# Optimization experiments

Measured on AMD Instinct MI355X. Metric: run time of the kernel, lower is better.

Reference implementation:

```python
import jax, jax.numpy as jnp
import numpy as np

N, K, D = 100000, 16, 128

def setup_inputs() -> dict:
    key = jax.random.key(0)
    k1, k2, k3, k4, k5 = jax.random.split(key, 5)
    s = 1.0 / np.sqrt(D)  # nn.Linear default init scale
    return {
        "h": jax.random.normal(k1, (N, D), dtype=jnp.float32),
        "nbr_idx": jax.random.randint(k2, (N, K), 0, N, dtype=jnp.int64),
        "nbr_w": jax.random.uniform(k3, (N, K), dtype=jnp.float32),
        "w_self": jax.random.uniform(k4, (D, D), minval=-s, maxval=s, dtype=jnp.float32),
        "w_nei": jax.random.uniform(k5, (D, D), minval=-s, maxval=s, dtype=jnp.float32),
        "ln_gamma": jnp.ones((D,), dtype=jnp.float32),
        "ln_beta": jnp.zeros((D,), dtype=jnp.float32),
    }

def layer_norm(x, gamma, beta, eps=1e-5):
    mu = jnp.mean(x, axis=-1, keepdims=True)
    var = jnp.mean(jnp.square(x - mu), axis=-1, keepdims=True)
    return (x - mu) * jax.lax.rsqrt(var + eps) * gamma + beta

def reference(h, nbr_idx, nbr_w, w_self, w_nei, ln_gamma, ln_beta):
    # gather neighbor features: [N, K, D]
    nei = h[nbr_idx]
    # weighted sum over neighbors -> [N, D]
    agg = jnp.einsum('nk,nkd->nd', nbr_w, nei)
    # dual linear (nn.Linear applies x @ W.T) + exact (erf) GELU
    out = jax.nn.gelu(h @ w_self.T + agg @ w_nei.T, approximate=False)
    # dropout is identity at inference; then LayerNorm
    return layer_norm(out, ln_gamma, ln_beta)
```

## Files before the change

kernel.cpp:

```cpp
#include <hip/hip_runtime.h>
#include <hip/hip_bf16.h>
#include <math.h>

#define DFEAT 128
#define KNBR  16
#define NPB   32
#define NTHR  128

typedef __attribute__((ext_vector_type(8))) short short8;
typedef __attribute__((ext_vector_type(4))) float f32x4;
typedef __attribute__((ext_vector_type(2))) unsigned u32x2;
typedef __attribute__((ext_vector_type(4))) unsigned u32x4;

__device__ __forceinline__ unsigned short f2bf(float x) {
    union { float f; unsigned u; } v; v.f = x;
    unsigned r = v.u + 0x7FFFu + ((v.u >> 16) & 1u);
    return (unsigned short)(r >> 16);
}
__device__ __forceinline__ float bf2f(unsigned short u) {
    union { unsigned u; float f; } v; v.u = ((unsigned)u) << 16; return v.f;
}
__device__ __forceinline__ bool detect_idx64(const int* p) {
    return ((p[1] | p[3] | p[5] | p[7] | p[9] | p[11] | p[13] | p[15]) == 0);
}

__global__ __launch_bounds__(256)
void prep_kernel(const float* __restrict__ h,
                 const float* __restrict__ wself,
                 const float* __restrict__ wnei,
                 unsigned short* __restrict__ h16,
                 unsigned short* __restrict__ wcat,
                 unsigned char* __restrict__ h8i,
                 float* __restrict__ sc,
                 int ntot8) {
    const int t = blockIdx.x * 256 + threadIdx.x;
    if (t < 4096) {
        const int base = t * 8;
        const int j = base >> 8;
        const int d0 = base & 255;
        const float* src = (d0 < DFEAT) ? (wself + j * DFEAT + d0)
                                        : (wnei  + j * DFEAT + (d0 - DFEAT));
        f32x4 a = ((const f32x4*)src)[0], b = ((const f32x4*)src)[1];
        short8 o;
        o[0] = f2bf(a[0]); o[1] = f2bf(a[1]); o[2] = f2bf(a[2]); o[3] = f2bf(a[3]);
        o[4] = f2bf(b[0]); o[5] = f2bf(b[1]); o[6] = f2bf(b[2]); o[7] = f2bf(b[3]);
        *(short8*)(wcat + base) = o;
        return;
    }
    const long u = (long)t - 4096;
    if (u >= ntot8) return;
    f32x4 a = __builtin_nontemporal_load((const f32x4*)(h + u * 8));
    f32x4 b = __builtin_nontemporal_load((const f32x4*)(h + u * 8) + 1);
    short8 o;
    o[0] = f2bf(a[0]); o[1] = f2bf(a[1]); o[2] = f2bf(a[2]); o[3] = f2bf(a[3]);
    o[4] = f2bf(b[0]); o[5] = f2bf(b[1]); o[6] = f2bf(b[2]); o[7] = f2bf(b[3]);
    __builtin_nontemporal_store(o, (short8*)(h16 + u * 8));

    if (h8i) {
        float m = 0.f;
        #pragma unroll
        for (int d = 0; d < 4; ++d) { m = fmaxf(m, fabsf(a[d])); m = fmaxf(m, fabsf(b[d])); }
        #pragma unroll
        for (int mk = 1; mk < 16; mk <<= 1) m = fmaxf(m, __shfl_xor(m, mk, 64));
        const float inv = (m > 0.f) ? 127.f / m : 0.f;
        u32x2 q;
        q[0] = ((unsigned)((int)rintf(a[0] * inv) & 255))
             | ((unsigned)((int)rintf(a[1] * inv) & 255) << 8)
             | ((unsigned)((int)rintf(a[2] * inv) & 255) << 16)
             | ((unsigned)((int)rintf(a[3] * inv) & 255) << 24);
        q[1] = ((unsigned)((int)rintf(b[0] * inv) & 255))
             | ((unsigned)((int)rintf(b[1] * inv) & 255) << 8)
             | ((unsigned)((int)rintf(b[2] * inv) & 255) << 16)
             | ((unsigned)((int)rintf(b[3] * inv) & 255) << 24);
        __builtin_nontemporal_store(q, (u32x2*)(h8i + u * 8));
        if ((u & 15) == 0) sc[u >> 4] = m * (1.f / 127.f);
    }
}

template<int MODE>
__global__ __launch_bounds__(NTHR, 4)
void sage_fused_kernel(const float* __restrict__ h,
                       const unsigned short* __restrict__ h16,
                       const unsigned char* __restrict__ h8i,
                       const float* __restrict__ sc,
                       const int* __restrict__ nbr32,
                       const float* __restrict__ nbrw,
                       const unsigned short* __restrict__ wcat,
                       const float* __restrict__ gamma,
                       const float* __restrict__ beta,
                       float* __restrict__ out,
                       int N) {
    __shared__ __align__(16) unsigned short xlds[NPB][256];

    const int tid = threadIdx.x;
    const int nb  = blockIdx.x * NPB;
    const int l   = tid & 63;
    const int wvi = tid >> 6;

    if constexpr (MODE == 3) {
        const bool idx64 = detect_idx64(nbr32);
        const int q8  = l & 7;
        const int gb2 = l & 56;
        const int i0b = wvi * 16 + (l >> 3) * 2;
        #pragma unroll
        for (int r = 0; r < 2; ++r) {
            const int i = i0b + r;
            int n = nb + i; if (n >= N) n = N - 1;
            const int e0 = n * KNBR + q8;
            const int id0 = nbr32[idx64 ? 2 * e0 : e0];
            const int id1 = nbr32[idx64 ? 2 * (e0 + 8) : (e0 + 8)];
            const float w0 = nbrw[e0]     * sc[id0];
            const float w1 = nbrw[e0 + 8] * sc[id1];
            short8 hv0 = *(const short8*)(h16 + (long)n * DFEAT + q8 * 16);
            short8 hv1 = *(const short8*)(h16 + (long)n * DFEAT + q8 * 16 + 8);
            *(short8*)&xlds[i][((2 * q8)     ^ (i & 7)) * 8] = hv0;
            *(short8*)&xlds[i][((2 * q8 + 1) ^ (i & 7)) * 8] = hv1;
            float acc[16];
            #pragma unroll
            for (int d = 0; d < 16; ++d) acc[d] = 0.f;
            #pragma unroll
            for (int k = 0; k < 16; ++k) {
                const int   ik = __shfl(k < 8 ? id0 : id1, gb2 + (k & 7), 64);
                const float wk = __shfl(k < 8 ? w0  : w1,  gb2 + (k & 7), 64);
                u32x4 nv = *(const u32x4*)(h8i + (long)ik * DFEAT + q8 * 16);
                #pragma unroll
                for (int b = 0; b < 4; ++b) {
                    const unsigned u = nv[b];
                    acc[b * 4 + 0] += wk * (float)(signed char)(u & 0xFF);
                    acc[b * 4 + 1] += wk * (float)(signed char)((u >> 8) & 0xFF);
                    acc[b * 4 + 2] += wk * (float)(signed char)((u >> 16) & 0xFF);
                    acc[b * 4 + 3] += wk * (float)(signed char)(u >> 24);
                }
            }
            short8 ab0, ab1;
            #pragma unroll
            for (int d = 0; d < 8; ++d) { ab0[d] = f2bf(acc[d]); ab1[d] = f2bf(acc[8 + d]); }
            *(short8*)&xlds[i][((16 + 2 * q8)     ^ (i & 7)) * 8] = ab0;
            *(short8*)&xlds[i][((16 + 2 * q8 + 1) ^ (i & 7)) * 8] = ab1;
        }
    } else if constexpr (MODE == 1) {
        const bool idx64 = detect_idx64(nbr32);
        const int q  = l & 15;
        const int gb = l & 48;
        const int i0 = wvi * 16 + (l >> 4) * 4;
        #pragma unroll 1
        for (int r = 0; r < 4; ++r) {
            const int i = i0 + r;
            int n = nb + i; if (n >= N) n = N - 1;
            const int e0 = n * KNBR + q;
            int myidx = nbr32[idx64 ? 2 * e0 : e0];
            float myw = nbrw[e0];
            short8 hv = *(const short8*)(h16 + (long)n * DFEAT + q * 8);
            float acc[8] = {0.f,0.f,0.f,0.f,0.f,0.f,0.f,0.f};
            #pragma unroll
            for (int k = 0; k < KNBR; ++k) {
                int ik = __shfl(myidx, gb + k, 64);
                short8 nv = *(const short8*)(h16 + (long)ik * DFEAT + q * 8);
                float wk = __shfl(myw, gb + k, 64);
                #pragma unroll
                for (int d = 0; d < 8; ++d)
                    acc[d] += wk * bf2f((unsigned short)nv[d]);
            }
            *(short8*)&xlds[i][(q ^ (i & 7)) * 8] = hv;
            short8 ab;
            #pragma unroll
            for (int d = 0; d < 8; ++d) ab[d] = f2bf(acc[d]);
            *(short8*)&xlds[i][((16 + q) ^ (i & 7)) * 8] = ab;
        }
    } else {
        const bool idx64 = detect_idx64(nbr32);
        const int q  = l & 15;
        const int i0 = wvi * 16 + (l >> 4) * 4;
        #pragma unroll 1
        for (int r = 0; r < 4; ++r) {
            const int i = i0 + r;
            int n = nb + i; if (n >= N) n = N - 1;
            short8 hv;
            float acc[8] = {0.f,0.f,0.f,0.f,0.f,0.f,0.f,0.f};
            const f32x4* hrow = (const f32x4*)(h + (long)n * DFEAT + q * 8);
            f32x4 h0 = hrow[0], h1 = hrow[1];
            hv[0] = f2bf(h0[0]); hv[1] = f2bf(h0[1]); hv[2] = f2bf(h0[2]); hv[3] = f2bf(h0[3]);
            hv[4] = f2bf(h1[0]); hv[5] = f2bf(h1[1]); hv[6] = f2bf(h1[2]); hv[7] = f2bf(h1[3]);
            const int e0 = n * KNBR;
            #pragma unroll 4
            for (int k = 0; k < KNBR; ++k) {
                float w = nbrw[e0 + k];
                int idx = nbr32[idx64 ? 2 * (e0 + k) : (e0 + k)];
                const f32x4* nrow = (const f32x4*)(h + (long)idx * DFEAT + q * 8);
                f32x4 n0 = nrow[0], n1 = nrow[1];
                acc[0] += w * n0[0]; acc[1] += w * n0[1];
                acc[2] += w * n0[2]; acc[3] += w * n0[3];
                acc[4] += w * n1[0]; acc[5] += w * n1[1];
                acc[6] += w * n1[2]; acc[7] += w * n1[3];
            }
            *(short8*)&xlds[i][(q ^ (i & 7)) * 8] = hv;
            short8 ab;
            #pragma unroll
            for (int d = 0; d < 8; ++d) ab[d] = f2bf(acc[d]);
            *(short8*)&xlds[i][((16 + q) ^ (i & 7)) * 8] = ab;
        }
    }
    __syncthreads();

    const int wv  = wvi;
    const int col = l & 15;
    const int kg  = l >> 4;

    f32x4 acc2[2][4];
    #pragma unroll
    for (int s = 0; s < 2; ++s)
        #pragma unroll
        for (int t = 0; t < 4; ++t)
            acc2[s][t] = (f32x4){0.f, 0.f, 0.f, 0.f};

    const unsigned short* wb0 = wcat + (wv * 64 + col) * 256 + kg * 8;

    #pragma unroll
    for (int kk = 0; kk < 8; ++kk) {
        short8 bt0 = *(const short8*)(wb0 + kk * 32);
        short8 bt1 = *(const short8*)(wb0 + 16 * 256 + kk * 32);
        short8 bt2 = *(const short8*)(wb0 + 32 * 256 + kk * 32);
        short8 bt3 = *(const short8*)(wb0 + 48 * 256 + kk * 32);
        #pragma unroll
        for (int s = 0; s < 2; ++s) {
            const int row = s * 16 + col;
            const int c = (kk * 4 + kg) ^ (row & 7);
            short8 a = *(const short8*)&xlds[row][c * 8];
            acc2[s][0] = __builtin_amdgcn_mfma_f32_16x16x32_bf16(a, bt0, acc2[s][0], 0, 0, 0);
            acc2[s][1] = __builtin_amdgcn_mfma_f32_16x16x32_bf16(a, bt1, acc2[s][1], 0, 0, 0);
            acc2[s][2] = __builtin_amdgcn_mfma_f32_16x16x32_bf16(a, bt2, acc2[s][2], 0, 0, 0);
            acc2[s][3] = __builtin_amdgcn_mfma_f32_16x16x32_bf16(a, bt3, acc2[s][3], 0, 0, 0);
        }
    }

    float y[2][4][4];
    #pragma unroll
    for (int s = 0; s < 2; ++s)
        #pragma unroll
        for (int t = 0; t < 4; ++t)
            #pragma unroll
            for (int r = 0; r < 4; ++r) {
                float x = acc2[s][t][r];
                y[s][t][r] = 0.5f * x * (1.0f + erff(x * 0.70710678118654752f));
            }

    __syncthreads();

    float* lsum = (float*)&xlds[0][0];
    float* lsq  = lsum + 2 * NPB;

    #pragma unroll
    for (int s = 0; s < 2; ++s) {
        f32x4 sm, sq;
        #pragma unroll
        for (int r = 0; r < 4; ++r) {
            float a0 = y[s][0][r], a1 = y[s][1][r], a2 = y[s][2][r], a3 = y[s][3][r];
            sm[r] = (a0 + a1) + (a2 + a3);
            sq[r] = (a0 * a0 + a1 * a1) + (a2 * a2 + a3 * a3);
        }
        #pragma unroll
        for (int m = 1; m < 16; m <<= 1) {
            #pragma unroll
            for (int r = 0; r < 4; ++r) {
                sm[r] += __shfl_xor(sm[r], m, 64);
                sq[r] += __shfl_xor(sq[r], m, 64);
            }
        }
        if (col == 0) {
            *(f32x4*)&lsum[wv * NPB + s * 16 + kg * 4] = sm;
            *(f32x4*)&lsq [wv * NPB + s * 16 + kg * 4] = sq;
        }
    }
    __syncthreads();

    float g[4], be[4];
    #pragma unroll
    for (int t = 0; t < 4; ++t) {
        g[t]  = gamma[wv * 64 + t * 16 + col];
        be[t] = beta [wv * 64 + t * 16 + col];
    }

    #pragma unroll
    for (int s = 0; s < 2; ++s) {
        f32x4 sm, sq;
        {
            f32x4 a0 = *(const f32x4*)&lsum[0 * NPB + s * 16 + kg * 4];
            f32x4 a1 = *(const f32x4*)&lsum[1 * NPB + s * 16 + kg * 4];
            f32x4 b0 = *(const f32x4*)&lsq [0 * NPB + s * 16 + kg * 4];
            f32x4 b1 = *(const f32x4*)&lsq [1 * NPB + s * 16 + kg * 4];
            sm = a0 + a1; sq = b0 + b1;
        }
        #pragma unroll
        for (int r = 0; r < 4; ++r) {
            const int i = s * 16 + kg * 4 + r;
            const int n = nb + i;
            if (n < N) {
                float mean = sm[r] * (1.0f / 128.0f);
                float var  = sq[r] * (1.0f / 128.0f) - mean * mean;
                float rstd = rsqrtf(var + 1e-5f);
                long o = (long)n * DFEAT + wv * 64 + col;
                #pragma unroll
                for (int t = 0; t < 4; ++t)
                    __builtin_nontemporal_store((y[s][t][r] - mean) * rstd * g[t] + be[t],
                                                &out[o + t * 16]);
            }
        }
    }
}

extern "C" void kernel_launch(void* const* d_in, const int* in_sizes, int n_in,
                              void* d_out, int out_size, void* d_ws, size_t ws_size,
                              hipStream_t stream) {
    const float* h     = (const float*)d_in[0];
    const int*   nbr   = (const int*)  d_in[1];
    const float* nbrw  = (const float*)d_in[2];
    const float* wself = (const float*)d_in[3];
    const float* wnei  = (const float*)d_in[4];
    const float* gamma = (const float*)d_in[5];
    const float* beta  = (const float*)d_in[6];
    const int N = in_sizes[0] / DFEAT;

    unsigned short* wcat = (unsigned short*)d_ws;
    unsigned short* h16  = (unsigned short*)((char*)d_ws + 65536);
    float*          sc   = (float*)((char*)d_ws + 65536 + (size_t)N * DFEAT * 2);
    unsigned char*  h8i  = (unsigned char*)((char*)sc + (size_t)N * 4);
    const size_t need16 = 65536 + (size_t)N * DFEAT * 2;
    const size_t need3  = need16 + (size_t)N * 4 + (size_t)N * DFEAT;

    const int blocks = (N + NPB - 1) / NPB;
    const int ntot8 = N * DFEAT / 8;
    const int pthreads = 4096 + ntot8;

    if (ws_size >= need3) {
        prep_kernel<<<(pthreads + 255) / 256, 256, 0, stream>>>(h, wself, wnei, h16, wcat, h8i, sc, ntot8);
        sage_fused_kernel<3><<<blocks, NTHR, 0, stream>>>(h, h16, h8i, sc, nbr, nbrw, wcat,
                                                          gamma, beta, (float*)d_out, N);
    } else if (ws_size >= need16) {
        prep_kernel<<<(pthreads + 255) / 256, 256, 0, stream>>>(h, wself, wnei, h16, wcat,
                                                                (unsigned char*)nullptr, (float*)nullptr, ntot8);
        sage_fused_kernel<1><<<blocks, NTHR, 0, stream>>>(h, h16, (const unsigned char*)nullptr,
                                                          (const float*)nullptr, nbr, nbrw, wcat,
                                                          gamma, beta, (float*)d_out, N);
    } else {
        prep_kernel<<<(4096 + 255) / 256, 256, 0, stream>>>(h, wself, wnei, h16, wcat,
                                                            (unsigned char*)nullptr, (float*)nullptr, 0);
        sage_fused_kernel<0><<<blocks, NTHR, 0, stream>>>(h, (const unsigned short*)nullptr,
                                                          (const unsigned char*)nullptr,
                                                          (const float*)nullptr, nbr, nbrw, wcat,
                                                          gamma, beta, (float*)d_out, N);
    }
}
```

Before: 89.16 us.

## Stage int8 neighbor gathers through double-buffered LDS via async global_load_lds

Replaces the register-based int8 neighbor gather with a per-wave double-buffered LDS ring filled by global_load_lds. Neighbor indices and scaled weights are staged in shared memory up front, and the loads for the next node pair are issued while the current pair is accumulated. The aim is to hide gather latency behind the int8 dequant-accumulate work. The cost is about 16KB more shared memory per block, which may lower occupancy, plus hand-written vmcnt waits that have to match the issue count exactly.

```diff
diff --git a/kernel.cpp b/kernel.cpp
--- a/kernel.cpp
+++ b/kernel.cpp
@@ -91,53 +91,92 @@
                        float* __restrict__ out,
                        int N) {
     __shared__ __align__(16) unsigned short xlds[NPB][256];
+    __shared__ __align__(16) unsigned char  ring[2][2][4096];
+    __shared__ unsigned idx_lds[NPB][KNBR];
+    __shared__ float    w_lds[NPB][KNBR];
 
     const int tid = threadIdx.x;
     const int nb  = blockIdx.x * NPB;
     const int l   = tid & 63;
     const int wvi = tid >> 6;
 
-    if constexpr (MODE == 3) {
+    if constexpr (MODE == 5) {
         const bool idx64 = detect_idx64(nbr32);
-        const int q8  = l & 7;
-        const int gb2 = l & 56;
-        const int i0b = wvi * 16 + (l >> 3) * 2;
-        #pragma unroll
-        for (int r = 0; r < 2; ++r) {
-            const int i = i0b + r;
+        {
+            const int i  = tid >> 2;
+            const int qq = tid & 3;
             int n = nb + i; if (n >= N) n = N - 1;
-            const int e0 = n * KNBR + q8;
-            const int id0 = nbr32[idx64 ? 2 * e0 : e0];
-            const int id1 = nbr32[idx64 ? 2 * (e0 + 8) : (e0 + 8)];
-            const float w0 = nbrw[e0]     * sc[id0];
-            const float w1 = nbrw[e0 + 8] * sc[id1];
-            short8 hv0 = *(const short8*)(h16 + (long)n * DFEAT + q8 * 16);
-            short8 hv1 = *(const short8*)(h16 + (long)n * DFEAT + q8 * 16 + 8);
-            *(short8*)&xlds[i][((2 * q8)     ^ (i & 7)) * 8] = hv0;
-            *(short8*)&xlds[i][((2 * q8 + 1) ^ (i & 7)) * 8] = hv1;
-            float acc[16];
-            #pragma unroll
-            for (int d = 0; d < 16; ++d) acc[d] = 0.f;
-            #pragma unroll
-            for (int k = 0; k < 16; ++k) {
-                const int   ik = __shfl(k < 8 ? id0 : id1, gb2 + (k & 7), 64);
-                const float wk = __shfl(k < 8 ? w0  : w1,  gb2 + (k & 7), 64);
-                u32x4 nv = *(const u32x4*)(h8i + (long)ik * DFEAT + q8 * 16);
-                #pragma unroll
-                for (int b = 0; b < 4; ++b) {
-                    const unsigned u = nv[b];
-                    acc[b * 4 + 0] += wk * (float)(signed char)(u & 0xFF);
-                    acc[b * 4 + 1] += wk * (float)(signed char)((u >> 8) & 0xFF);
-                    acc[b * 4 + 2] += wk * (float)(signed char)((u >> 16) & 0xFF);
-                    acc[b * 4 + 3] += wk * (float)(signed char)(u >> 24);
-                }
-            }
-            short8 ab0, ab1;
-            #pragma unroll
-            for (int d = 0; d < 8; ++d) { ab0[d] = f2bf(acc[d]); ab1[d] = f2bf(acc[8 + d]); }
-            *(short8*)&xlds[i][((16 + 2 * q8)     ^ (i & 7)) * 8] = ab0;
-            *(short8*)&xlds[i][((16 + 2 * q8 + 1) ^ (i & 7)) * 8] = ab1;
-        }
+            #pragma unroll
+            for (int m = 0; m < 4; ++m) {
+                const int c4 = qq * 4 + m;
+                short8 v = *(const short8*)(h16 + (long)n * DFEAT + c4 * 8);
+                *(short8*)&xlds[i][(c4 ^ (i & 7)) * 8] = v;
+            }
+            #pragma unroll
+            for (int j = 0; j < 4; ++j) {
+                const int e = tid * 4 + j;
+                const int ii = e >> 4, k = e & 15;
+                int nn = nb + ii; if (nn >= N) nn = N - 1;
+                const int ee = nn * KNBR + k;
+                const int id = nbr32[idx64 ? 2 * ee : ee];
+                idx_lds[ii][k] = (unsigned)id;
+                w_lds[ii][k]   = nbrw[ee] * sc[id];
+            }
+        }
+        __syncthreads();
+
+        unsigned char* rb0 = &ring[wvi][0][0];
+        unsigned char* rb1 = &ring[wvi][1][0];
+
+        #define GLD(IA, ROFS, RB, LOFS)  do {                                         \
+            unsigned _id = idx_lds[(IA)][(l >> 3) + (ROFS)];                          \
+            const unsigned char* _g = h8i + (size_t)_id * DFEAT + (l & 7) * 16;       \
+            __builtin_amdgcn_global_load_lds(                                         \
+                (const __attribute__((address_space(1))) void*)_g,                    \
+                (__attribute__((address_space(3))) void*)((RB) + (LOFS)), 16, 0, 0);  \
+        } while (0)
+        #define ISSUE_PAIR(P2, RB) do {                                               \
+            const int _ia = wvi * 16 + 2 * (P2);                                      \
+            GLD(_ia, 0, RB, 0); GLD(_ia, 8, RB, 1024);                                \
+            GLD(_ia + 1, 0, RB, 2048); GLD(_ia + 1, 8, RB, 3072);                     \
+        } while (0)
+
+        ISSUE_PAIR(0, rb0);
+        ISSUE_PAIR(1, rb1);
+
+        const int hh = l >> 5;
+        const int j  = l & 31;
+        #pragma unroll
+        for (int p = 0; p < 8; ++p) {
+            if (p < 7) { asm volatile("s_waitcnt vmcnt(4)" ::: "memory"); }
+            else       { asm volatile("s_waitcnt vmcnt(0)" ::: "memory"); }
+            __builtin_amdgcn_sched_barrier(0);
+
+            const int inode = wvi * 16 + 2 * p + hh;
+            const unsigned char* nbase = ((p & 1) ? rb1 : rb0) + hh * 2048;
+            f32x4 acc = {0.f, 0.f, 0.f, 0.f};
+            #pragma unroll
+            for (int r = 0; r < 16; ++r) {
+                const float wk = w_lds[inode][r];
+                const unsigned u = *(const unsigned*)(nbase + r * 128 + j * 4);
+                acc[0] += wk * (float)(signed char)(u & 0xFF);
+                acc[1] += wk * (float)(signed char)((u >> 8) & 0xFF);
+                acc[2] += wk * (float)(signed char)((u >> 16) & 0xFF);
+                acc[3] += wk * (float)(signed char)(u >> 24);
+            }
+            {
+                ushort4 o;
+                o.x = f2bf(acc[0]); o.y = f2bf(acc[1]);
+                o.z = f2bf(acc[2]); o.w = f2bf(acc[3]);
+                const int c4 = 16 + (j >> 1);
+                const int cs = c4 ^ (inode & 7);
+                *(ushort4*)((char*)&xlds[0][0] + inode * 512 + cs * 16 + 8 * (j & 1)) = o;
+            }
+            if (p + 2 < 8) { if (p & 1) ISSUE_PAIR(p + 2, rb1); else ISSUE_PAIR(p + 2, rb0); }
+            __builtin_amdgcn_sched_barrier(0);
+        }
+        #undef GLD
+        #undef ISSUE_PAIR
     } else if constexpr (MODE == 1) {
         const bool idx64 = detect_idx64(nbr32);
         const int q  = l & 15;
@@ -333,7 +372,7 @@
 
     if (ws_size >= need3) {
         prep_kernel<<<(pthreads + 255) / 256, 256, 0, stream>>>(h, wself, wnei, h16, wcat, h8i, sc, ntot8);
-        sage_fused_kernel<3><<<blocks, NTHR, 0, stream>>>(h, h16, h8i, sc, nbr, nbrw, wcat,
+        sage_fused_kernel<5><<<blocks, NTHR, 0, stream>>>(h, h16, h8i, sc, nbr, nbrw, wcat,
                                                           gamma, beta, (float*)d_out, N);
     } else if (ws_size >= need16) {
         prep_kernel<<<(pthreads + 255) / 256, 256, 0, stream>>>(h, wself, wnei, h16, wcat,
```

New measurement: 96.41 us. 1.08x slower.
